# Optimization experiments

Hardware: AMD Instinct MI355X
Metric: run time of the kernel (lower is better)

## Reference

```python
import jax, jax.numpy as jnp
import numpy as np

IN_F, OUT_F, GS = 4096, 11008, 128


def setup_inputs() -> dict:
    key = jax.random.key(0)
    k1, k2, k3, k4 = jax.random.split(key, 4)
    x = jax.random.normal(k1, (4, 2048, IN_F), dtype=jnp.float32)
    # int8-valued weights stored in int32 container, as in the module
    weight = jax.random.randint(k2, (OUT_F, IN_F), -128, 128, dtype=jnp.int32)
    # scales in [...,0] (kept positive-ish), zeros in [...,1]
    scales = jax.random.uniform(k3, (IN_F // GS, OUT_F, 1), dtype=jnp.float32, minval=0.001, maxval=0.02)
    zeros = jax.random.normal(k4, (IN_F // GS, OUT_F, 1), dtype=jnp.float32) * 0.1
    scales_and_zeros = jnp.concatenate([scales, zeros], axis=-1)
    bias = jax.random.normal(jax.random.fold_in(key, 7), (OUT_F,), dtype=jnp.float32) * 0.02
    return {"x": x, "weight": weight, "scales_and_zeros": scales_and_zeros, "bias": bias, "group_size": GS}


def reference(x, weight, scales_and_zeros, bias, group_size):
    O, I = weight.shape
    G = I // group_size
    orig_shape = x.shape
    x2 = x.reshape(-1, I)                                   # [N, I]
    scales = scales_and_zeros[:, :, 0]                      # [G, O]
    zeros = scales_and_zeros[:, :, 1]                       # [G, O]
    # per-group dequant: w_fp[o, g, j] = q * scale[g, o] + zero[g, o]
    wq = weight.reshape(O, G, group_size).astype(x.dtype)   # [O, G, gs]
    w_fp = wq * scales.T[:, :, None] + zeros.T[:, :, None]  # [O, G, gs]
    w_fp = w_fp.reshape(O, I)
    y = x2 @ w_fp.T + bias                                  # [N, O]
    return y.reshape(*orig_shape[:-1], O)
```

## Files before the change

kernel.cpp:

```cpp
#include <hip/hip_runtime.h>
#include <stdint.h>

#define DEVFN __device__ __forceinline__

constexpr int M_DIM = 8192;
constexpr int K_DIM = 4096;
constexpr int N_DIM = 11008;
constexpr int GS = 128;
constexpr int NGROUPS = K_DIM / GS;

typedef __bf16 bf16_t;
typedef bf16_t bf16x8 __attribute__((ext_vector_type(8)));
typedef float f32x4 __attribute__((ext_vector_type(4)));

DEVFN ushort f2bf(float f) {
  uint32_t u = __builtin_bit_cast(uint32_t, f);
  u += 0x7fffu + ((u >> 16) & 1u);
  return (ushort)(u >> 16);
}

__global__ __launch_bounds__(256) void k_cvt_x(const float* __restrict__ x,
                                               ushort* __restrict__ out) {
  const size_t i4 = (size_t)blockIdx.x * 256 + threadIdx.x;
  const float4 v = ((const float4*)x)[i4];
  ushort4 r;
  r.x = f2bf(v.x); r.y = f2bf(v.y); r.z = f2bf(v.z); r.w = f2bf(v.w);
  ((ushort4*)out)[i4] = r;
}

__global__ __launch_bounds__(256) void k_dequant_w(const int* __restrict__ w,
                                                   const float* __restrict__ snz,
                                                   ushort* __restrict__ out) {
  const size_t i4 = (size_t)blockIdx.x * 256 + threadIdx.x;
  const size_t idx = i4 * 4;
  const int o = (int)(idx >> 12);
  const int i = (int)(idx & 4095);
  const int g = i >> 7;
  const float2 sz = ((const float2*)snz)[(size_t)g * N_DIM + o];
  const int4 wv = ((const int4*)w)[i4];
  ushort4 r;
  r.x = f2bf((float)wv.x * sz.x + sz.y);
  r.y = f2bf((float)wv.y * sz.x + sz.y);
  r.z = f2bf((float)wv.z * sz.x + sz.y);
  r.w = f2bf((float)wv.w * sz.x + sz.y);
  ((ushort4*)out)[i4] = r;
}

constexpr int BM2 = 256, BN2 = 256, BK2 = 64;
constexpr int NBM2 = M_DIM / BM2;
constexpr int NBN2 = N_DIM / BN2;
constexpr int KT2 = K_DIM / BK2;
constexpr int NWG2 = NBM2 * NBN2;

#define BAR() __builtin_amdgcn_s_barrier()
#define LGKM0() asm volatile("s_waitcnt lgkmcnt(0)" ::: "memory")
#define VMC4() asm volatile("s_waitcnt vmcnt(4)" ::: "memory")
#define VMC0() asm volatile("s_waitcnt vmcnt(0)" ::: "memory")

DEVFN void gld16(const ushort* g, ushort* l) {
  __builtin_amdgcn_global_load_lds(
      (const __attribute__((address_space(1))) void*)g,
      (__attribute__((address_space(3))) void*)l, 16, 0, 0);
}

DEVFN void stage_half(const ushort* gbase, int h, int kt, ushort* lp) {
  const ushort* s = gbase + (size_t)(h * 128) * K_DIM + kt * 64;
  gld16(s, lp);
  gld16(s + (size_t)64 * K_DIM, lp + 4096);
}

template <int H>
DEVFN void lda(const ushort* p0, const ushort* p1, bf16x8 (&af)[4][2]) {
#pragma unroll
  for (int mi = 0; mi < 4; ++mi) {
    af[mi][0] = *(const bf16x8*)(p0 + (H * 4 + mi) * 1024);
    af[mi][1] = *(const bf16x8*)(p1 + (H * 4 + mi) * 1024);
  }
}
template <int P>
DEVFN void ldb(const ushort* p0, const ushort* p1, bf16x8 (&bv)[4][2]) {
#pragma unroll
  for (int q = 0; q < 2; ++q) {
    bv[P * 2 + q][0] = *(const bf16x8*)(p0 + (P * 2 + q) * 1024);
    bv[P * 2 + q][1] = *(const bf16x8*)(p1 + (P * 2 + q) * 1024);
  }
}
template <int H, int P>
DEVFN void mm16(f32x4 (&acc)[8][4], const bf16x8 (&af)[4][2], const bf16x8 (&bv)[4][2]) {
#pragma unroll
  for (int kk = 0; kk < 2; ++kk)
#pragma unroll
    for (int mi = 0; mi < 4; ++mi)
#pragma unroll
      for (int ni = 0; ni < 2; ++ni)
        acc[H * 4 + mi][P * 2 + ni] = __builtin_amdgcn_mfma_f32_16x16x32_bf16(
            af[mi][kk], bv[P * 2 + ni][kk], acc[H * 4 + mi][P * 2 + ni], 0, 0, 0);
}

__global__ __launch_bounds__(512) void k_gemm256(const ushort* __restrict__ A,
                                                 const ushort* __restrict__ B,
                                                 const float* __restrict__ bias,
                                                 float* __restrict__ C) {
  __shared__ __align__(16) ushort smem[65536];

  const int tid = threadIdx.x;
  const int wave = tid >> 6;
  const int lane = tid & 63;
  const int wm = wave >> 2;
  const int wn = wave & 3;
  const int fr = lane & 15;
  const int quad = lane >> 4;
  const int frq = fr & 7;

  const int bid = blockIdx.x;
  const int wg = (bid & 7) * (NWG2 / 8) + (bid >> 3);
  const int bm = wg / NBN2;
  const int bn = wg - bm * NBN2;

  const int ch0 = ((quad ^ frq) << 3);
  const int ch1 = (((4 | quad) ^ frq) << 3);
  const ushort* pA00 = smem + (wm * 128 + fr) * 64 + ch0;
  const ushort* pA01 = smem + (wm * 128 + fr) * 64 + ch1;
  const ushort* pA10 = pA00 + 32768;
  const ushort* pA11 = pA01 + 32768;
  const ushort* pB00 = smem + 16384 + (wn * 64 + fr) * 64 + ch0;
  const ushort* pB01 = smem + 16384 + (wn * 64 + fr) * 64 + ch1;
  const ushort* pB10 = pB00 + 32768;
  const ushort* pB11 = pB01 + 32768;

  const int srow = tid >> 3;
  const int scol = ((tid & 7) ^ (srow & 7)) * 8;
  const ushort* pAg = A + (size_t)(bm * 256 + srow) * K_DIM + scol;
  const ushort* pBg = B + (size_t)(bn * 256 + srow) * K_DIM + scol;
  ushort* const ws = smem + wave * 512;

  f32x4 acc[8][4] = {};

  stage_half(pAg, 0, 0, ws + 0);
  stage_half(pAg, 1, 0, ws + 8192);
  stage_half(pBg, 0, 0, ws + 16384);
  stage_half(pBg, 1, 0, ws + 24576);
  stage_half(pBg, 0, 1, ws + 49152);
  stage_half(pBg, 1, 1, ws + 57344);
  VMC4();
  BAR();

#pragma unroll 1
  for (int it = 0; it < KT2 / 2; ++it) {
    const int t1 = 2 * it + 1;
    const int t2 = (2 * it + 2 < KT2) ? 2 * it + 2 : KT2 - 1;
    const int t3 = (2 * it + 3 < KT2) ? 2 * it + 3 : KT2 - 1;
    bf16x8 af[4][2], bv[4][2];
    lda<0>(pA00, pA01, af);
    ldb<0>(pB00, pB01, bv);
    stage_half(pAg, 0, t1, ws + 32768);
    BAR(); LGKM0();
    __builtin_amdgcn_s_setprio(1); mm16<0, 0>(acc, af, bv); __builtin_amdgcn_s_setprio(0);
    BAR();
    ldb<1>(pB00, pB01, bv);
    stage_half(pAg, 1, t1, ws + 40960);
    BAR(); LGKM0();
    __builtin_amdgcn_s_setprio(1); mm16<0, 1>(acc, af, bv); __builtin_amdgcn_s_setprio(0);
    BAR();
    lda<1>(pA00, pA01, af);
    stage_half(pBg, 0, t2, ws + 16384);
    BAR(); LGKM0();
    __builtin_amdgcn_s_setprio(1); mm16<1, 1>(acc, af, bv); __builtin_amdgcn_s_setprio(0);
    BAR();
    stage_half(pBg, 1, t2, ws + 24576);
    BAR();
    __builtin_amdgcn_s_setprio(1); mm16<1, 0>(acc, af, bv); __builtin_amdgcn_s_setprio(0);
    VMC4();
    BAR();
    lda<0>(pA10, pA11, af);
    ldb<0>(pB10, pB11, bv);
    stage_half(pAg, 0, t2, ws + 0);
    BAR(); LGKM0();
    __builtin_amdgcn_s_setprio(1); mm16<0, 0>(acc, af, bv); __builtin_amdgcn_s_setprio(0);
    BAR();
    ldb<1>(pB10, pB11, bv);
    stage_half(pAg, 1, t2, ws + 8192);
    BAR(); LGKM0();
    __builtin_amdgcn_s_setprio(1); mm16<0, 1>(acc, af, bv); __builtin_amdgcn_s_setprio(0);
    BAR();
    lda<1>(pA10, pA11, af);
    stage_half(pBg, 0, t3, ws + 49152);
    BAR(); LGKM0();
    __builtin_amdgcn_s_setprio(1); mm16<1, 1>(acc, af, bv); __builtin_amdgcn_s_setprio(0);
    BAR();
    stage_half(pBg, 1, t3, ws + 57344);
    BAR();
    __builtin_amdgcn_s_setprio(1); mm16<1, 0>(acc, af, bv); __builtin_amdgcn_s_setprio(0);
    VMC4();
    BAR();
  }
  VMC0();

  const int row0 = bm * 256 + wm * 128 + quad * 4;
  const int col0 = bn * 256 + wn * 64 + fr;
#pragma unroll
  for (int ni = 0; ni < 4; ++ni) {
    const int col = col0 + ni * 16;
    const float bvv = bias[col];
#pragma unroll
    for (int mi = 0; mi < 8; ++mi) {
      float* cp = C + (size_t)(row0 + mi * 16) * N_DIM + col;
#pragma unroll
      for (int r = 0; r < 4; ++r)
        cp[(size_t)r * N_DIM] = acc[mi][ni][r] + bvv;
    }
  }
}

__global__ __launch_bounds__(256) void k_naive(const float* __restrict__ x,
                                               const int* __restrict__ w,
                                               const float* __restrict__ snz,
                                               const float* __restrict__ bias,
                                               float* __restrict__ y) {
  const int o = blockIdx.x * 256 + threadIdx.x;
  const int m = blockIdx.y;
  const float* xr = x + (size_t)m * K_DIM;
  const int* wr = w + (size_t)o * K_DIM;
  float acc = 0.f;
  for (int g = 0; g < NGROUPS; ++g) {
    const float2 sz = ((const float2*)snz)[(size_t)g * N_DIM + o];
    float pd = 0.f, px = 0.f;
    const int base = g * GS;
    for (int i = 0; i < GS; i += 4) {
      float4 xv = *(const float4*)(xr + base + i);
      int4 wv = *(const int4*)(wr + base + i);
      pd += xv.x * wv.x + xv.y * wv.y + xv.z * wv.z + xv.w * wv.w;
      px += xv.x + xv.y + xv.z + xv.w;
    }
    acc += sz.x * pd + sz.y * px;
  }
  y[(size_t)m * N_DIM + o] = acc + bias[o];
}

extern "C" void kernel_launch(void* const* d_in, const int* in_sizes, int n_in,
                              void* d_out, int out_size, void* d_ws, size_t ws_size,
                              hipStream_t stream) {
  const float* x    = (const float*)d_in[0];
  const int*   w    = (const int*)d_in[1];
  const float* snz  = (const float*)d_in[2];
  const float* bias = (const float*)d_in[3];
  float* out = (float*)d_out;

  const size_t wbytes = (size_t)N_DIM * K_DIM * 2;
  const size_t xbytes = (size_t)M_DIM * K_DIM * 2;

  if (ws_size >= wbytes + xbytes) {
    ushort* wbf = (ushort*)d_ws;
    ushort* xbf = (ushort*)((char*)d_ws + wbytes);
    k_cvt_x<<<dim3(32768), dim3(256), 0, stream>>>(x, xbf);
    k_dequant_w<<<dim3(44032), dim3(256), 0, stream>>>(w, snz, wbf);
    k_gemm256<<<dim3(NWG2), dim3(512), 0, stream>>>(xbf, wbf, bias, out);
  } else {
    k_naive<<<dim3(N_DIM / 256, M_DIM), dim3(256), 0, stream>>>(x, w, snz, bias, out);
  }
}
```

Measured before the change: 1.155 ms.

## Software-pipeline LDS fragment loads behind MFMA and halve barriers in GEMM loop

Restructures the main K loop so each LDS fragment load for the next MFMA block is issued right after the current MFMA block. This overlaps LDS reads with matrix math and removes the explicit lgkmcnt(0) waits and about half of the s_barriers. Fragment registers are hoisted out of the loop and preloaded before it. The vmcnt waits are tightened to 2 at different points, and launch bounds now request 2 blocks per CU. Relying on the compiler to insert the LDS waits and on reordered barriers risks read-after-write hazards on the LDS buffers, and the occupancy hint may force register spills.

Result: no change. 1.138 ms (-1.4%).

```diff
diff --git a/kernel.cpp b/kernel.cpp
--- a/kernel.cpp
+++ b/kernel.cpp
@@ -52,10 +52,12 @@
 constexpr int KT2 = K_DIM / BK2;
 constexpr int NWG2 = NBM2 * NBN2;
 
-#define BAR() __builtin_amdgcn_s_barrier()
-#define LGKM0() asm volatile("s_waitcnt lgkmcnt(0)" ::: "memory")
+#define BARM() asm volatile("s_barrier" ::: "memory")
+#define VMC2() asm volatile("s_waitcnt vmcnt(2)" ::: "memory")
 #define VMC4() asm volatile("s_waitcnt vmcnt(4)" ::: "memory")
 #define VMC0() asm volatile("s_waitcnt vmcnt(0)" ::: "memory")
+#define PRIO1() __builtin_amdgcn_s_setprio(1)
+#define PRIO0() __builtin_amdgcn_s_setprio(0)
 
 DEVFN void gld16(const ushort* g, ushort* l) {
   __builtin_amdgcn_global_load_lds(
@@ -97,10 +99,10 @@
             af[mi][kk], bv[P * 2 + ni][kk], acc[H * 4 + mi][P * 2 + ni], 0, 0, 0);
 }
 
-__global__ __launch_bounds__(512) void k_gemm256(const ushort* __restrict__ A,
-                                                 const ushort* __restrict__ B,
-                                                 const float* __restrict__ bias,
-                                                 float* __restrict__ C) {
+__global__ __launch_bounds__(512, 2) void k_gemm256(const ushort* __restrict__ A,
+                                                    const ushort* __restrict__ B,
+                                                    const float* __restrict__ bias,
+                                                    float* __restrict__ C) {
   __shared__ __align__(16) ushort smem[65536];
 
   const int tid = threadIdx.x;
@@ -135,6 +137,7 @@
   ushort* const ws = smem + wave * 512;
 
   f32x4 acc[8][4] = {};
+  bf16x8 af[4][2], bv[4][2];
 
   stage_half(pAg, 0, 0, ws + 0);
   stage_half(pAg, 1, 0, ws + 8192);
@@ -143,56 +146,49 @@
   stage_half(pBg, 0, 1, ws + 49152);
   stage_half(pBg, 1, 1, ws + 57344);
   VMC4();
-  BAR();
+  BARM();
+  lda<0>(pA00, pA01, af);
+  ldb<0>(pB00, pB01, bv);
 
 #pragma unroll 1
   for (int it = 0; it < KT2 / 2; ++it) {
     const int t1 = 2 * it + 1;
     const int t2 = (2 * it + 2 < KT2) ? 2 * it + 2 : KT2 - 1;
     const int t3 = (2 * it + 3 < KT2) ? 2 * it + 3 : KT2 - 1;
-    bf16x8 af[4][2], bv[4][2];
+    stage_half(pAg, 0, t1, ws + 32768);
+    PRIO1(); mm16<0, 0>(acc, af, bv); PRIO0();
+    ldb<1>(pB00, pB01, bv);
+    BARM();
+    stage_half(pAg, 1, t1, ws + 40960);
+    PRIO1(); mm16<0, 1>(acc, af, bv); PRIO0();
+    lda<1>(pA00, pA01, af);
+    BARM();
+    stage_half(pBg, 0, t2, ws + 16384);
+    PRIO1(); mm16<1, 1>(acc, af, bv); PRIO0();
+    VMC2();
+    BARM();
+    stage_half(pBg, 1, t2, ws + 24576);
+    PRIO1(); mm16<1, 0>(acc, af, bv); PRIO0();
+    lda<0>(pA10, pA11, af);
+    ldb<0>(pB10, pB11, bv);
+    BARM();
+    stage_half(pAg, 0, t2, ws + 0);
+    PRIO1(); mm16<0, 0>(acc, af, bv); PRIO0();
+    ldb<1>(pB10, pB11, bv);
+    BARM();
+    stage_half(pAg, 1, t2, ws + 8192);
+    PRIO1(); mm16<0, 1>(acc, af, bv); PRIO0();
+    lda<1>(pA10, pA11, af);
+    BARM();
+    stage_half(pBg, 0, t3, ws + 49152);
+    PRIO1(); mm16<1, 1>(acc, af, bv); PRIO0();
+    VMC2();
+    BARM();
+    stage_half(pBg, 1, t3, ws + 57344);
+    PRIO1(); mm16<1, 0>(acc, af, bv); PRIO0();
     lda<0>(pA00, pA01, af);
     ldb<0>(pB00, pB01, bv);
-    stage_half(pAg, 0, t1, ws + 32768);
-    BAR(); LGKM0();
-    __builtin_amdgcn_s_setprio(1); mm16<0, 0>(acc, af, bv); __builtin_amdgcn_s_setprio(0);
-    BAR();
-    ldb<1>(pB00, pB01, bv);
-    stage_half(pAg, 1, t1, ws + 40960);
-    BAR(); LGKM0();
-    __builtin_amdgcn_s_setprio(1); mm16<0, 1>(acc, af, bv); __builtin_amdgcn_s_setprio(0);
-    BAR();
-    lda<1>(pA00, pA01, af);
-    stage_half(pBg, 0, t2, ws + 16384);
-    BAR(); LGKM0();
-    __builtin_amdgcn_s_setprio(1); mm16<1, 1>(acc, af, bv); __builtin_amdgcn_s_setprio(0);
-    BAR();
-    stage_half(pBg, 1, t2, ws + 24576);
-    BAR();
-    __builtin_amdgcn_s_setprio(1); mm16<1, 0>(acc, af, bv); __builtin_amdgcn_s_setprio(0);
-    VMC4();
-    BAR();
-    lda<0>(pA10, pA11, af);
-    ldb<0>(pB10, pB11, bv);
-    stage_half(pAg, 0, t2, ws + 0);
-    BAR(); LGKM0();
-    __builtin_amdgcn_s_setprio(1); mm16<0, 0>(acc, af, bv); __builtin_amdgcn_s_setprio(0);
-    BAR();
-    ldb<1>(pB10, pB11, bv);
-    stage_half(pAg, 1, t2, ws + 8192);
-    BAR(); LGKM0();
-    __builtin_amdgcn_s_setprio(1); mm16<0, 1>(acc, af, bv); __builtin_amdgcn_s_setprio(0);
-    BAR();
-    lda<1>(pA10, pA11, af);
-    stage_half(pBg, 0, t3, ws + 49152);
-    BAR(); LGKM0();
-    __builtin_amdgcn_s_setprio(1); mm16<1, 1>(acc, af, bv); __builtin_amdgcn_s_setprio(0);
-    BAR();
-    stage_half(pBg, 1, t3, ws + 57344);
-    BAR();
-    __builtin_amdgcn_s_setprio(1); mm16<1, 0>(acc, af, bv); __builtin_amdgcn_s_setprio(0);
-    VMC4();
-    BAR();
+    BARM();
   }
   VMC0();
 
```
